# Kernel tuning notes

Hardware: AMD Instinct MI355X
Metric: run time of the kernel (lower is better)

## Reference

```python
import jax, jax.numpy as jnp
import numpy as np

H = 16
HD = 128
ROPE_BASE = 10000.0

def _rope_cos_sin(T, dtype):
    inv_freq = 1.0 / (ROPE_BASE ** (jnp.arange(0, HD, 2, dtype=jnp.float32) / HD))  # [HD/2]
    pos = jnp.arange(T, dtype=jnp.float32)
    freqs = pos[:, None] * inv_freq[None, :]  # [T, HD/2]
    return jnp.cos(freqs).astype(dtype), jnp.sin(freqs).astype(dtype)

def _apply_rotary(x, cos, sin):
    # x: [B,H,T,HD]; cos/sin: [T,HD/2]
    x1, x2 = x[..., : HD // 2], x[..., HD // 2 :]
    c = cos[None, None, :, :]
    s = sin[None, None, :, :]
    return jnp.concatenate([x1 * c - x2 * s, x1 * s + x2 * c], axis=-1)

def setup_inputs() -> dict:
    key = jax.random.key(0)
    ks = jax.random.split(key, 5)
    B, T, D = 2, 2048, 2048
    x = jax.random.normal(ks[0], (B, T, D), dtype=jnp.float32)
    Wqkv = jax.random.normal(ks[1], (3 * D, D), dtype=jnp.float32) * (D ** -0.5)
    bqkv = jax.random.normal(ks[2], (3 * D,), dtype=jnp.float32) * 0.02
    Wo = jax.random.normal(ks[3], (D, D), dtype=jnp.float32) * (D ** -0.5)
    bo = jax.random.normal(ks[4], (D,), dtype=jnp.float32) * 0.02
    # causal mask: True = masked (future positions)
    mask = jnp.triu(jnp.ones((T, T), dtype=bool), k=1)[None, None, :, :]
    return {"x": x, "Wqkv": Wqkv, "bqkv": bqkv, "Wo": Wo, "bo": bo, "mask": mask}

def reference(x, Wqkv, bqkv, Wo, bo, mask):
    B, T, D = x.shape
    qkv = x @ Wqkv.T + bqkv  # [B,T,3D]
    q, k, v = jnp.split(qkv, 3, axis=-1)
    def to_heads(t):
        return t.reshape(B, T, H, HD).transpose(0, 2, 1, 3)  # [B,H,T,HD]
    q, k, v = to_heads(q), to_heads(k), to_heads(v)
    cos, sin = _rope_cos_sin(T, x.dtype)
    q = _apply_rotary(q, cos, sin)
    k = _apply_rotary(k, cos, sin)
    scale = HD ** 0.5
    attn = jnp.einsum('bhqd,bhkd->bhqk', q, k) / scale
    neg = -jnp.finfo(x.dtype).max
    attn = jnp.where(mask, neg, attn)
    w = jax.nn.softmax(attn, axis=-1)
    out = jnp.einsum('bhqk,bhkd->bhqd', w, v)  # [B,H,T,HD]
    out = out.transpose(0, 2, 1, 3).reshape(B, T, H * HD)
    return out @ Wo.T + bo
```

## Files before the change

kernel.cpp:

```cpp
#include <hip/hip_runtime.h>
#include <hip/hip_bf16.h>
#include <cstdint>

typedef __bf16 bf16;
typedef __bf16 bf16x8 __attribute__((ext_vector_type(8)));
typedef float  f32x4  __attribute__((ext_vector_type(4)));

#define B_   2
#define T_   2048
#define D_   2048
#define H_   16
#define HD_  128

typedef __attribute__((address_space(3))) void       lds_void;
typedef __attribute__((address_space(1))) const void gbl_void;
__device__ __forceinline__ void glds16(const bf16* g, bf16* l) {
    __builtin_amdgcn_global_load_lds((gbl_void*)g, (lds_void*)l, 16, 0, 0);
}

__device__ __forceinline__ ushort4 cvt4(const float4 v) {
    union { bf16 h[4]; ushort4 u; } pk;
    pk.h[0] = (bf16)v.x; pk.h[1] = (bf16)v.y;
    pk.h[2] = (bf16)v.z; pk.h[3] = (bf16)v.w;
    return pk.u;
}

__global__ __launch_bounds__(256) void convert_xw_kernel(
    const float* __restrict__ x, const float* __restrict__ wqkv,
    bf16* __restrict__ xb, bf16* __restrict__ wqkvb)
{
    const int NX = (B_ * T_ * D_) / 4;
    const int NT = NX + (3 * D_ * D_) / 4;
    for (int g = blockIdx.x * blockDim.x + threadIdx.x; g < NT;
         g += gridDim.x * blockDim.x) {
        if (g < NX) ((ushort4*)xb)[g]      = cvt4(((const float4*)x)[g]);
        else        ((ushort4*)wqkvb)[g-NX] = cvt4(((const float4*)wqkv)[g-NX]);
    }
}

__global__ __launch_bounds__(256) void convert_wo_kernel(
    const float* __restrict__ wo, bf16* __restrict__ wob)
{
    const int N = (D_ * D_) / 4;
    for (int g = blockIdx.x * blockDim.x + threadIdx.x; g < N;
         g += gridDim.x * blockDim.x)
        ((ushort4*)wob)[g] = cvt4(((const float4*)wo)[g]);
}

__device__ __forceinline__ void gemm_core_glds(
    const bf16* __restrict__ A, const bf16* __restrict__ W, int K,
    int bm, int bn, int tid, f32x4 (&acc)[4][4],
    bf16* lds_a, bf16* lds_b)
{
    const int lane = tid & 63, quad = lane >> 4, lcol = lane & 15;
    const int wave = tid >> 6;
    const int wm = (wave >> 1) * 64, wn2 = (wave & 1) * 32;
    const int sw = lcol & 7;
    const int sr = tid >> 3, pc = tid & 7;
    const int sc = (pc ^ (sr & 7)) * 8;
    const bf16* abase = A + (size_t)(bm * 128 + sr) * K + sc;
    const bf16* bbase = W + (size_t)(bn * 128 + sr) * K + sc;
    bf16* la = lds_a + sr * 64 + pc * 8;
    bf16* lb = lds_b + sr * 64 + pc * 8;

    for (int k0 = 0; k0 < K; k0 += 64) {
        __syncthreads();
#pragma unroll
        for (int p = 0; p < 4; p++) {
            glds16(abase + k0 + (size_t)32 * p * K, la + 2048 * p);
            glds16(bbase + k0 + (size_t)32 * p * K, lb + 2048 * p);
        }
        __syncthreads();
#pragma unroll
        for (int kk = 0; kk < 2; kk++) {
            bf16x8 af[4], bfr[4];
#pragma unroll
            for (int i = 0; i < 4; i++)
                af[i] = *(const bf16x8*)&lds_a[(wm + i * 16 + lcol) * 64 +
                                               (((kk * 4 + quad) ^ sw) * 8)];
#pragma unroll
            for (int j = 0; j < 4; j++) {
                const int row = wn2 + (j & 1) * 16 + (j >> 1) * 64 + lcol;
                bfr[j] = *(const bf16x8*)&lds_b[row * 64 +
                                                (((kk * 4 + quad) ^ sw) * 8)];
            }
#pragma unroll
            for (int i = 0; i < 4; i++)
#pragma unroll
                for (int j = 0; j < 4; j++)
                    acc[i][j] = __builtin_amdgcn_mfma_f32_16x16x32_bf16(af[i], bfr[j], acc[i][j], 0, 0, 0);
        }
    }
}

__global__ __launch_bounds__(256) void qkv_gemm_kernel(
    const bf16* __restrict__ xb, const bf16* __restrict__ wqkvb,
    const float* __restrict__ bias,
    bf16* __restrict__ qh, bf16* __restrict__ kh, bf16* __restrict__ vT)
{
    __shared__ bf16 lds_a[128 * 64];
    __shared__ bf16 lds_b[128 * 64];
    const int tid = threadIdx.x;
    const int bm = blockIdx.y, bn = blockIdx.x;
    const int lane = tid & 63, quad = lane >> 4, lcol = lane & 15;
    const int wave = tid >> 6;
    const int wm = (wave >> 1) * 64, wn2 = (wave & 1) * 32;

    f32x4 acc[4][4];
    const f32x4 z = {0.f, 0.f, 0.f, 0.f};
#pragma unroll
    for (int i = 0; i < 4; i++)
#pragma unroll
        for (int j = 0; j < 4; j++) acc[i][j] = z;

    gemm_core_glds(xb, wqkvb, D_, bm, bn, tid, acc, lds_a, lds_b);

    const int n0 = bn * 128;
    const int part = bn / 16;
    const int h = bn & 15;
    const int mb0 = bm * 128 + wm;

    if (part < 2) {
        bf16* dst = (part == 0) ? qh : kh;
#pragma unroll
        for (int i = 0; i < 4; i++) {
#pragma unroll
            for (int jp = 0; jp < 2; jp++) {
                const int d1 = wn2 + jp * 16 + lcol;
                const float invf = __expf(-0.14391156831212787f * (float)d1);
                const float b1 = bias[n0 + d1];
                const float b2 = bias[n0 + d1 + 64];
#pragma unroll
                for (int r = 0; r < 4; r++) {
                    const int m = mb0 + i * 16 + quad * 4 + r;
                    const int bb = m >> 11, t = m & (T_ - 1);
                    const float x1 = acc[i][jp][r] + b1;
                    const float x2 = acc[i][jp + 2][r] + b2;
                    float s, c;
                    __sincosf((float)t * invf, &s, &c);
                    const size_t rowo = ((size_t)(bb * H_ + h) * T_ + t) * HD_;
                    dst[rowo + d1]      = (bf16)(x1 * c - x2 * s);
                    dst[rowo + d1 + 64] = (bf16)(x1 * s + x2 * c);
                }
            }
        }
    } else {
        const int bb = mb0 >> 11, t64 = mb0 & (T_ - 1);
        const int bh = bb * H_ + h;
#pragma unroll
        for (int j = 0; j < 4; j++) {
            const int d = wn2 + (j & 1) * 16 + (j >> 1) * 64 + lcol;
            const float bv = bias[n0 + d];
            bf16* vdst = &vT[((size_t)bh * HD_ + d) * T_ + t64];
#pragma unroll
            for (int r = 0; r < 4; r++) {
                union { bf16 hh[4]; ushort4 u; } pk;
#pragma unroll
                for (int i = 0; i < 4; i++) pk.hh[i] = (bf16)(acc[i][j][r] + bv);
                *(ushort4*)&vdst[(quad * 4 + r) * 4] = pk.u;
            }
        }
    }
}

__global__ __launch_bounds__(256, 2) void attn_kernel(
    const bf16* __restrict__ qh, const bf16* __restrict__ kh,
    const bf16* __restrict__ vT, bf16* __restrict__ ctx)
{
    __shared__ bf16 lds_k[2][64 * 128];
    __shared__ bf16 lds_v[2][128 * 64];
    __shared__ bf16 lds_p[128 * 64];
    const int tid = threadIdx.x;
    const int id = blockIdx.x;
    const int bh = id & 31;
    const int q4 = (id >> 5) & 7;
    const int qt = (id >> 8) ? (15 - q4) : q4;
    const int q0 = qt * 128;
    const int lane = tid & 63, quad = lane >> 4, lcol = lane & 15;
    const int wave = tid >> 6;
    const int wq0 = wave * 32;
    const float scale2 = 0.08838834764831845f * 1.4426950408889634f;

    const bf16* kbase = kh + (size_t)bh * T_ * HD_;
    const bf16* vbase = vT + (size_t)bh * HD_ * T_;

    const int ksrow = tid >> 4;
    const bf16* kstage = kbase + (size_t)ksrow * HD_ + (((tid & 15) ^ ksrow) << 3);
    const int vsd = tid >> 3;
    const bf16* vstage = vbase + (size_t)vsd * T_ + (((tid & 7) ^ (vsd & 7)) << 3);

    bf16x8 qf[2][4];
#pragma unroll
    for (int i = 0; i < 2; i++)
#pragma unroll
        for (int kk = 0; kk < 4; kk++)
            qf[i][kk] = *(const bf16x8*)&qh[((size_t)bh * T_ + q0 + wq0 + i * 16 + lcol) * HD_ +
                                            kk * 32 + quad * 8];

    f32x4 o[2][8];
    const f32x4 z = {0.f, 0.f, 0.f, 0.f};
#pragma unroll
    for (int i = 0; i < 2; i++)
#pragma unroll
        for (int jd = 0; jd < 8; jd++) o[i][jd] = z;
    float l_part[2][4];
#pragma unroll
    for (int i = 0; i < 2; i++)
#pragma unroll
        for (int r = 0; r < 4; r++) l_part[i][r] = 0.f;

    const int wrow_min = q0 + wq0;
    const int wrow_max = wrow_min + 31;

    const int ktmax = 2 * qt + 2;
#pragma unroll
    for (int p = 0; p < 4; p++) {
        glds16(kstage + (size_t)16 * p * HD_, &lds_k[0][tid * 8 + p * 2048]);
        glds16(vstage + (size_t)32 * p * T_, &lds_v[0][tid * 8 + p * 2048]);
    }

    for (int kt = 0; kt < ktmax; kt++) {
        __syncthreads();
        if (kt + 1 < ktmax) {
            const bf16* ks = kstage + (size_t)(kt + 1) * 64 * HD_;
            const bf16* vs = vstage + (kt + 1) * 64;
            bf16* lkd = &lds_k[(kt + 1) & 1][tid * 8];
            bf16* lvd = &lds_v[(kt + 1) & 1][tid * 8];
#pragma unroll
            for (int p = 0; p < 4; p++) {
                glds16(ks + (size_t)16 * p * HD_, lkd + p * 2048);
                glds16(vs + (size_t)32 * p * T_, lvd + p * 2048);
            }
        }
        if (kt * 64 > wrow_max) continue;
        const bool needmask = (kt * 64 + 63 > wrow_min);
        const bf16* lk = lds_k[kt & 1];
        const bf16* lv = lds_v[kt & 1];

        f32x4 s_acc[2][4];
#pragma unroll
        for (int i = 0; i < 2; i++)
#pragma unroll
            for (int j = 0; j < 4; j++) s_acc[i][j] = z;
        __builtin_amdgcn_s_setprio(1);
#pragma unroll
        for (int kk = 0; kk < 4; kk++) {
#pragma unroll
            for (int j = 0; j < 4; j++) {
                const bf16x8 bk = *(const bf16x8*)&lk[(j * 16 + lcol) * 128 +
                                        (((kk * 4 + quad) ^ lcol) << 3)];
#pragma unroll
                for (int i = 0; i < 2; i++)
                    s_acc[i][j] = __builtin_amdgcn_mfma_f32_16x16x32_bf16(qf[i][kk], bk, s_acc[i][j], 0, 0, 0);
            }
        }
        __builtin_amdgcn_s_setprio(0);

#pragma unroll
        for (int i = 0; i < 2; i++) {
#pragma unroll
            for (int r = 0; r < 4; r++) {
                const int prow = wq0 + i * 16 + quad * 4 + r;
                const int qrow = q0 + prow;
                union { bf16 hh[4]; ushort4 u; } pk;
                float lp = 0.f;
#pragma unroll
                for (int j = 0; j < 4; j++) {
                    float p = exp2f(fmaf(s_acc[i][j][r], scale2, -16.0f));
                    if (needmask) {
                        const int kcol = kt * 64 + j * 16 + lcol;
                        p = (kcol > qrow) ? 0.f : p;
                    }
                    lp += p;
                    pk.hh[j] = (bf16)p;
                }
                l_part[i][r] += lp;
                *(ushort4*)&lds_p[prow * 64 + ((lcol * 4) ^ ((prow & 7) << 3))] = pk.u;
            }
        }

#pragma unroll
        for (int kk2 = 0; kk2 < 2; kk2++) {
            bf16x8 pf[2], vf[8];
#pragma unroll
            for (int i = 0; i < 2; i++) {
                const int prow = wq0 + i * 16 + lcol;
                pf[i] = *(const bf16x8*)&lds_p[prow * 64 +
                            ((kk2 * 32 + quad * 8) ^ ((lcol & 7) << 3))];
            }
#pragma unroll
            for (int jd = 0; jd < 8; jd++) {
                const int d = jd * 16 + lcol;
                vf[jd] = *(const bf16x8*)&lv[d * 64 +
                              (((kk2 * 4 + quad) ^ (lcol & 7)) << 3)];
            }
            __builtin_amdgcn_s_setprio(1);
#pragma unroll
            for (int i = 0; i < 2; i++)
#pragma unroll
                for (int jd = 0; jd < 8; jd++)
                    o[i][jd] = __builtin_amdgcn_mfma_f32_16x16x32_bf16(pf[i], vf[jd], o[i][jd], 0, 0, 0);
            __builtin_amdgcn_s_setprio(0);
        }
    }

    float inv_l[2][4];
#pragma unroll
    for (int i = 0; i < 2; i++)
#pragma unroll
        for (int r = 0; r < 4; r++) {
            float rs = l_part[i][r];
#pragma unroll
            for (int off = 1; off < 16; off <<= 1)
                rs += __shfl_xor(rs, off);
            inv_l[i][r] = 1.0f / rs;
        }
    const int b = bh >> 4, h = bh & 15;
#pragma unroll
    for (int i = 0; i < 2; i++) {
#pragma unroll
        for (int r = 0; r < 4; r++) {
            const int t = q0 + wq0 + i * 16 + quad * 4 + r;
#pragma unroll
            for (int jd = 0; jd < 8; jd++)
                ctx[((size_t)(b * T_ + t)) * D_ + h * HD_ + jd * 16 + lcol] =
                    (bf16)(o[i][jd][r] * inv_l[i][r]);
        }
    }
}

__global__ __launch_bounds__(256) void proj_gemm_kernel(
    const bf16* __restrict__ ctx, const bf16* __restrict__ wob,
    const float* __restrict__ bias, float* __restrict__ out)
{
    __shared__ bf16 lds_a[128 * 64];
    __shared__ bf16 lds_b[128 * 64];
    const int tid = threadIdx.x;
    const int bm = blockIdx.y, bn = blockIdx.x;
    const int lane = tid & 63, quad = lane >> 4, lcol = lane & 15;
    const int wave = tid >> 6;
    const int wm = (wave >> 1) * 64, wn2 = (wave & 1) * 32;

    f32x4 acc[4][4];
    const f32x4 z = {0.f, 0.f, 0.f, 0.f};
#pragma unroll
    for (int i = 0; i < 4; i++)
#pragma unroll
        for (int j = 0; j < 4; j++) acc[i][j] = z;

    gemm_core_glds(ctx, wob, D_, bm, bn, tid, acc, lds_a, lds_b);

    const int n0 = bn * 128;
#pragma unroll
    for (int i = 0; i < 4; i++) {
#pragma unroll
        for (int j = 0; j < 4; j++) {
            const int n = n0 + wn2 + (j & 1) * 16 + (j >> 1) * 64 + lcol;
            const float bv = bias[n];
#pragma unroll
            for (int r = 0; r < 4; r++) {
                const int m = bm * 128 + wm + i * 16 + quad * 4 + r;
                out[(size_t)m * D_ + n] = acc[i][j][r] + bv;
            }
        }
    }
}

extern "C" void kernel_launch(void* const* d_in, const int* in_sizes, int n_in,
                              void* d_out, int out_size, void* d_ws, size_t ws_size,
                              hipStream_t stream)
{
    const float* x    = (const float*)d_in[0];
    const float* Wqkv = (const float*)d_in[1];
    const float* bqkv = (const float*)d_in[2];
    const float* Wo   = (const float*)d_in[3];
    const float* bo   = (const float*)d_in[4];
    float* out = (float*)d_out;

    const size_t HT = (size_t)B_ * H_ * T_ * HD_;
    bf16* xb   = (bf16*)d_ws;
    bf16* qh   = xb + HT;
    bf16* kh   = qh + HT;
    bf16* vT   = kh + HT;
    bf16* ctx  = xb;
    bf16* wob  = qh;
    bf16* wqkvb = (bf16*)d_out;

    convert_xw_kernel<<<2560, 256, 0, stream>>>(x, Wqkv, xb, wqkvb);
    qkv_gemm_kernel<<<dim3(48, 32), 256, 0, stream>>>(xb, wqkvb, bqkv, qh, kh, vT);
    attn_kernel<<<512, 256, 0, stream>>>(qh, kh, vT, ctx);
    convert_wo_kernel<<<1024, 256, 0, stream>>>(Wo, wob);
    proj_gemm_kernel<<<dim3(16, 32), 256, 0, stream>>>(ctx, wob, bo, out);
}
```

Before: 374.2 us.

## Pair complementary causal query tiles per attention block for load balance

Each attention block now handles two query tiles, qt and 15-qt, one after the other in a single pipelined loop of 36 K/V tile steps. This gives every block the same amount of causal work and keeps the K/V prefetch running across the switch between tiles. The grid is halved to 256 blocks and the launch bound drops to one block per SM, which frees registers but lowers occupancy. On a GPU with many CUs, 256 blocks may leave some CUs idle.

```diff
diff --git a/kernel.cpp b/kernel.cpp
--- a/kernel.cpp
+++ b/kernel.cpp
@@ -163,7 +163,7 @@
     }
 }
 
-__global__ __launch_bounds__(256, 2) void attn_kernel(
+__global__ __launch_bounds__(256, 1) void attn_kernel(
     const bf16* __restrict__ qh, const bf16* __restrict__ kh,
     const bf16* __restrict__ vT, bf16* __restrict__ ctx)
 {
@@ -173,13 +173,15 @@
     const int tid = threadIdx.x;
     const int id = blockIdx.x;
     const int bh = id & 31;
-    const int q4 = (id >> 5) & 7;
-    const int qt = (id >> 8) ? (15 - q4) : q4;
-    const int q0 = qt * 128;
+    const int qp = id >> 5;
+    const int qtA = 15 - qp;
+    const int qtB = qp;
+    const int ktA = 2 * qtA + 2;
     const int lane = tid & 63, quad = lane >> 4, lcol = lane & 15;
     const int wave = tid >> 6;
     const int wq0 = wave * 32;
     const float scale2 = 0.08838834764831845f * 1.4426950408889634f;
+    const int b = bh >> 4, h = bh & 15;
 
     const bf16* kbase = kh + (size_t)bh * T_ * HD_;
     const bf16* vbase = vT + (size_t)bh * HD_ * T_;
@@ -189,13 +191,18 @@
     const int vsd = tid >> 3;
     const bf16* vstage = vbase + (size_t)vsd * T_ + (((tid & 7) ^ (vsd & 7)) << 3);
 
+    int q0 = qtA * 128;
+
     bf16x8 qf[2][4];
-#pragma unroll
-    for (int i = 0; i < 2; i++)
-#pragma unroll
-        for (int kk = 0; kk < 4; kk++)
-            qf[i][kk] = *(const bf16x8*)&qh[((size_t)bh * T_ + q0 + wq0 + i * 16 + lcol) * HD_ +
-                                            kk * 32 + quad * 8];
+    auto load_q = [&](int q0_) {
+#pragma unroll
+        for (int i = 0; i < 2; i++)
+#pragma unroll
+            for (int kk = 0; kk < 4; kk++)
+                qf[i][kk] = *(const bf16x8*)&qh[((size_t)bh * T_ + q0_ + wq0 + i * 16 + lcol) * HD_ +
+                                                kk * 32 + quad * 8];
+    };
+    load_q(q0);
 
     f32x4 o[2][8];
     const f32x4 z = {0.f, 0.f, 0.f, 0.f};
@@ -209,33 +216,74 @@
 #pragma unroll
         for (int r = 0; r < 4; r++) l_part[i][r] = 0.f;
 
-    const int wrow_min = q0 + wq0;
-    const int wrow_max = wrow_min + 31;
-
-    const int ktmax = 2 * qt + 2;
+    auto do_epilogue = [&](int q0_) {
+        float inv_l[2][4];
+#pragma unroll
+        for (int i = 0; i < 2; i++)
+#pragma unroll
+            for (int r = 0; r < 4; r++) {
+                float rs = l_part[i][r];
+#pragma unroll
+                for (int off = 1; off < 16; off <<= 1)
+                    rs += __shfl_xor(rs, off);
+                inv_l[i][r] = 1.0f / rs;
+            }
+#pragma unroll
+        for (int i = 0; i < 2; i++) {
+#pragma unroll
+            for (int r = 0; r < 4; r++) {
+                const int t = q0_ + wq0 + i * 16 + quad * 4 + r;
+#pragma unroll
+                for (int jd = 0; jd < 8; jd++)
+                    ctx[((size_t)(b * T_ + t)) * D_ + h * HD_ + jd * 16 + lcol] =
+                        (bf16)(o[i][jd][r] * inv_l[i][r]);
+            }
+        }
+    };
+
+    int wrow_min = q0 + wq0;
+    int wrow_max = wrow_min + 31;
+
 #pragma unroll
     for (int p = 0; p < 4; p++) {
         glds16(kstage + (size_t)16 * p * HD_, &lds_k[0][tid * 8 + p * 2048]);
         glds16(vstage + (size_t)32 * p * T_, &lds_v[0][tid * 8 + p * 2048]);
     }
 
-    for (int kt = 0; kt < ktmax; kt++) {
+    for (int s = 0; s < 36; s++) {
         __syncthreads();
-        if (kt + 1 < ktmax) {
-            const bf16* ks = kstage + (size_t)(kt + 1) * 64 * HD_;
-            const bf16* vs = vstage + (kt + 1) * 64;
-            bf16* lkd = &lds_k[(kt + 1) & 1][tid * 8];
-            bf16* lvd = &lds_v[(kt + 1) & 1][tid * 8];
+        if (s + 1 < 36) {
+            const int kn = (s + 1 < ktA) ? (s + 1) : (s + 1 - ktA);
+            const bf16* ks = kstage + (size_t)kn * 64 * HD_;
+            const bf16* vs = vstage + kn * 64;
+            bf16* lkd = &lds_k[(s + 1) & 1][tid * 8];
+            bf16* lvd = &lds_v[(s + 1) & 1][tid * 8];
 #pragma unroll
             for (int p = 0; p < 4; p++) {
                 glds16(ks + (size_t)16 * p * HD_, lkd + p * 2048);
                 glds16(vs + (size_t)32 * p * T_, lvd + p * 2048);
             }
         }
+        if (s == ktA) {
+            do_epilogue(q0);
+            q0 = qtB * 128;
+            load_q(q0);
+#pragma unroll
+            for (int i = 0; i < 2; i++)
+#pragma unroll
+                for (int jd = 0; jd < 8; jd++) o[i][jd] = z;
+#pragma unroll
+            for (int i = 0; i < 2; i++)
+#pragma unroll
+                for (int r = 0; r < 4; r++) l_part[i][r] = 0.f;
+            wrow_min = q0 + wq0;
+            wrow_max = wrow_min + 31;
+        }
+        const int kt = (s < ktA) ? s : (s - ktA);
         if (kt * 64 > wrow_max) continue;
         const bool needmask = (kt * 64 + 63 > wrow_min);
-        const bf16* lk = lds_k[kt & 1];
-        const bf16* lv = lds_v[kt & 1];
+        const bf16* lk = lds_k[s & 1];
+        const bf16* lv = lds_v[s & 1];
 
         f32x4 s_acc[2][4];
 #pragma unroll
@@ -304,29 +352,7 @@
         }
     }
 
-    float inv_l[2][4];
-#pragma unroll
-    for (int i = 0; i < 2; i++)
-#pragma unroll
-        for (int r = 0; r < 4; r++) {
-            float rs = l_part[i][r];
-#pragma unroll
-            for (int off = 1; off < 16; off <<= 1)
-                rs += __shfl_xor(rs, off);
-            inv_l[i][r] = 1.0f / rs;
-        }
-    const int b = bh >> 4, h = bh & 15;
-#pragma unroll
-    for (int i = 0; i < 2; i++) {
-#pragma unroll
-        for (int r = 0; r < 4; r++) {
-            const int t = q0 + wq0 + i * 16 + quad * 4 + r;
-#pragma unroll
-            for (int jd = 0; jd < 8; jd++)
-                ctx[((size_t)(b * T_ + t)) * D_ + h * HD_ + jd * 16 + lcol] =
-                    (bf16)(o[i][jd][r] * inv_l[i][r]);
-        }
-    }
+    do_epilogue(q0);
 }
 
 __global__ __launch_bounds__(256) void proj_gemm_kernel(
@@ -388,7 +414,7 @@
 
     convert_xw_kernel<<<2560, 256, 0, stream>>>(x, Wqkv, xb, wqkvb);
     qkv_gemm_kernel<<<dim3(48, 32), 256, 0, stream>>>(xb, wqkvb, bqkv, qh, kh, vT);
-    attn_kernel<<<512, 256, 0, stream>>>(qh, kh, vT, ctx);
+    attn_kernel<<<256, 256, 0, stream>>>(qh, kh, vT, ctx);
     convert_wo_kernel<<<1024, 256, 0, stream>>>(Wo, wob);
     proj_gemm_kernel<<<dim3(16, 32), 256, 0, stream>>>(ctx, wob, bo, out);
 }
```

Result: slower. 388.6 us (+3.9%).
